# Performance work log

Measured on AMD Instinct MI355X. Metric: run time of the kernel, lower is better.

The kernel has to match this reference:

```python
import jax, jax.numpy as jnp
import numpy as np

N = 100000
E = 1600000
D_IN = 128
HEADS = 8
HEAD_DIM = 16  # hidden_channels // heads = 128 // 8
D_HID = HEADS * HEAD_DIM  # 128
D_OUT = 128
NEG_SLOPE = 0.2


def setup_inputs() -> dict:
    key = jax.random.key(0)
    ks = jax.random.split(key, 10)
    x = jax.random.normal(ks[0], (N, D_IN), dtype=jnp.float32)
    edge_index = jax.random.randint(ks[1], (2, E), 0, N, dtype=jnp.int64)
    s = 1.0 / np.sqrt(D_IN)
    W_gat = jax.random.uniform(ks[2], (D_IN, D_HID), minval=-s, maxval=s, dtype=jnp.float32)
    att_src = jax.random.uniform(ks[3], (HEADS, HEAD_DIM), minval=-s, maxval=s, dtype=jnp.float32)
    att_dst = jax.random.uniform(ks[4], (HEADS, HEAD_DIM), minval=-s, maxval=s, dtype=jnp.float32)
    b_gat = jnp.zeros((D_HID,), dtype=jnp.float32)
    so = 1.0 / np.sqrt(D_OUT)
    W_fc1 = jax.random.uniform(ks[5], (D_OUT, D_OUT), minval=-so, maxval=so, dtype=jnp.float32)
    b_fc1 = jax.random.uniform(ks[6], (D_OUT,), minval=-so, maxval=so, dtype=jnp.float32)
    W_fc2 = jax.random.uniform(ks[7], (D_OUT, D_OUT), minval=-so, maxval=so, dtype=jnp.float32)
    b_fc2 = jax.random.uniform(ks[8], (D_OUT,), minval=-so, maxval=so, dtype=jnp.float32)
    return {"x": x, "edge_index": edge_index, "W_gat": W_gat, "att_src": att_src,
            "att_dst": att_dst, "b_gat": b_gat, "W_fc1": W_fc1, "b_fc1": b_fc1,
            "W_fc2": W_fc2, "b_fc2": b_fc2}


def _gat_conv(x, src, dst, W_gat, att_src, att_dst, b_gat):
    n = x.shape[0]
    xp = (x @ W_gat).reshape(n, HEADS, HEAD_DIM)        # [N,H,C]
    a_src = jnp.einsum('nhc,hc->nh', xp, att_src)       # [N,H]
    a_dst = jnp.einsum('nhc,hc->nh', xp, att_dst)       # [N,H]
    e = jax.nn.leaky_relu(a_src[src] + a_dst[dst], NEG_SLOPE)  # [E,H]
    # segment softmax over edges grouped by destination node
    e_max = jax.ops.segment_max(e, dst, num_segments=n)
    e = jnp.exp(e - e_max[dst])
    e_sum = jax.ops.segment_sum(e, dst, num_segments=n)
    alpha = e / (e_sum[dst] + 1e-16)                    # [E,H]
    msg = xp[src] * alpha[:, :, None]                   # [E,H,C]
    out = jax.ops.segment_sum(msg, dst, num_segments=n) # [N,H,C]
    return out.reshape(n, D_HID) + b_gat


def reference(x, edge_index, W_gat, att_src, att_dst, b_gat, W_fc1, b_fc1, W_fc2, b_fc2):
    n = x.shape[0]
    # PyG GATConv default add_self_loops=True
    loops = jnp.arange(n, dtype=edge_index.dtype)
    src = jnp.concatenate([edge_index[0], loops])
    dst = jnp.concatenate([edge_index[1], loops])
    z = _gat_conv(x, src, dst, W_gat, att_src, att_dst, b_gat)
    z1 = z @ W_fc1 + b_fc1
    z2 = z @ W_fc2 + b_fc2
    return (z, z1, z2)
```

## Files before the change

kernel.cpp:

```cpp
#include <hip/hip_runtime.h>
#include <hip/hip_bf16.h>


#define NBUCK  256
#define BSHIFT 9
#define BNODES 512
#define IPB    8192

typedef __attribute__((ext_vector_type(8))) short bf16x8;
typedef __attribute__((ext_vector_type(4))) float f32x4;

static __device__ __forceinline__ short f2bf(float f) {
    __hip_bfloat16 h = __float2bfloat16(f);
    return *reinterpret_cast<short*>(&h);
}

__global__ __launch_bounds__(256) void k0_swizzle(
    const float* __restrict__ W0, const float* __restrict__ W1,
    const float* __restrict__ W2, unsigned short* __restrict__ S0,
    unsigned short* __restrict__ S1, unsigned short* __restrict__ S2)
{
    const int t = blockIdx.x * 256 + threadIdx.x;
    if (t >= 3 * 2048) return;
    const int m = t >> 11;
    const int r = t & 2047;
    const int tile = r >> 6;
    const int l    = r & 63;
    const int ks   = tile & 3;
    const int cb   = tile >> 2;
    const int c    = cb * 16 + (l & 15);
    const int kb   = ks * 32 + (l >> 4) * 8;
    const float* W = (m == 0) ? W0 : (m == 1) ? W1 : W2;
    unsigned short* S = (m == 0) ? S0 : (m == 1) ? S1 : S2;
    unsigned short* dst = S + ((size_t)tile * 64 + l) * 8;
#pragma unroll
    for (int j = 0; j < 8; ++j)
        dst[j] = (unsigned short)f2bf(W[(kb + j) * 128 + c]);
}

__global__ __launch_bounds__(256) void g1_mfma(
    const float* __restrict__ x, const unsigned short* __restrict__ Wswz,
    unsigned short* __restrict__ xpb, int n)
{
    const int wid  = __builtin_amdgcn_readfirstlane(threadIdx.x >> 6);
    const int lane = threadIdx.x & 63;
    const int lr   = lane & 15;
    const int kg   = lane >> 4;
    const int rowbase = blockIdx.x * 128 + wid * 32;

    bf16x8 afr[2][4];
#pragma unroll
    for (int rt = 0; rt < 2; ++rt) {
        int row = rowbase + rt * 16 + lr;
        row = (row < n) ? row : (n - 1);
        const float* rp = x + (size_t)row * 128 + kg * 8;
#pragma unroll
        for (int ks = 0; ks < 4; ++ks) {
            const float4 v0 = *reinterpret_cast<const float4*>(rp + ks * 32);
            const float4 v1 = *reinterpret_cast<const float4*>(rp + ks * 32 + 4);
            bf16x8 a;
            a[0] = f2bf(v0.x); a[1] = f2bf(v0.y); a[2] = f2bf(v0.z); a[3] = f2bf(v0.w);
            a[4] = f2bf(v1.x); a[5] = f2bf(v1.y); a[6] = f2bf(v1.z); a[7] = f2bf(v1.w);
            afr[rt][ks] = a;
        }
    }

    f32x4 acc[2][8] = {};
#pragma unroll
    for (int cb = 0; cb < 8; ++cb) {
        const unsigned short* bp = Wswz + ((size_t)(cb * 4) * 64 + lane) * 8;
        bf16x8 bfr[4];
#pragma unroll
        for (int ks = 0; ks < 4; ++ks)
            bfr[ks] = *reinterpret_cast<const bf16x8*>(bp + (size_t)ks * 512);
#pragma unroll
        for (int ks = 0; ks < 4; ++ks) {
            acc[0][cb] = __builtin_amdgcn_mfma_f32_16x16x32_bf16(afr[0][ks], bfr[ks], acc[0][cb], 0, 0, 0);
            acc[1][cb] = __builtin_amdgcn_mfma_f32_16x16x32_bf16(afr[1][ks], bfr[ks], acc[1][cb], 0, 0, 0);
        }
    }

#pragma unroll
    for (int rt = 0; rt < 2; ++rt) {
#pragma unroll
        for (int reg = 0; reg < 4; ++reg) {
            const int row = rowbase + rt * 16 + kg * 4 + reg;
            if (row < n) {
                unsigned short* op = xpb + (size_t)row * 128 + lr;
#pragma unroll
                for (int cb = 0; cb < 8; ++cb)
                    op[cb * 16] = (unsigned short)f2bf(acc[rt][cb][reg]);
            }
        }
    }
}

__global__ __launch_bounds__(256) void k1b_att(
    const unsigned short* __restrict__ xpb, const float* __restrict__ att_s,
    const float* __restrict__ att_d, float* __restrict__ a_src,
    float* __restrict__ a_dst, int n)
{
    const int tid  = threadIdx.x;
    const int col  = tid & 127;
    const int half = __builtin_amdgcn_readfirstlane(tid >> 7);
    const int rb   = blockIdx.x * 32 + half * 16;
    if (rb >= n) return;
    const float asw = att_s[col];
    const float adw = att_d[col];
    const int h = col >> 4;
#pragma unroll 4
    for (int r = 0; r < 16; ++r) {
        const int row = rb + r;
        if (row >= n) break;
        const unsigned int u = (unsigned int)xpb[(size_t)row * 128 + col] << 16;
        const float v = __uint_as_float(u);
        float sv = v * asw;
        float dv = v * adw;
#pragma unroll
        for (int off = 1; off < 16; off <<= 1) {
            sv += __shfl_xor(sv, off);
            dv += __shfl_xor(dv, off);
        }
        if ((col & 15) == 0) {
            a_src[row * 8 + h] = sv;
            a_dst[row * 8 + h] = dv;
        }
    }
}

__global__ __launch_bounds__(256) void p1_hist(
    const int* __restrict__ ei, int* __restrict__ M, int E, int N, int nblk)
{
    __shared__ int h[NBUCK];
    const int tid = threadIdx.x;
    for (int k = tid; k < NBUCK; k += 256) h[k] = 0;
    __syncthreads();

    const int tot = E + N;
    const int base = blockIdx.x * IPB;
    const int lim = (base + IPB < tot) ? base + IPB : tot;
    for (int j = base + tid; j < lim; j += 256) {
        const int d = (j < E) ? ei[E + j] : (j - E);
        atomicAdd(&h[d >> BSHIFT], 1);
    }
    __syncthreads();
    for (int k = tid; k < NBUCK; k += 256)
        M[(size_t)k * nblk + blockIdx.x] = h[k];
}

__global__ __launch_bounds__(256) void p2a_colscan(
    int* __restrict__ M, int* __restrict__ col_total, int nblk)
{
    const int b    = blockIdx.x;
    const int tid  = threadIdx.x;
    const int lane = tid & 63;
    const int wid  = tid >> 6;
    __shared__ int wsum[4];

    int carry = 0;
    for (int base = 0; base < nblk; base += 256) {
        const int idx = base + tid;
        const int v = (idx < nblk) ? M[(size_t)b * nblk + idx] : 0;
        int ws = v;
#pragma unroll
        for (int off = 1; off < 64; off <<= 1) {
            const int t = __shfl_up(ws, off);
            if (lane >= off) ws += t;
        }
        if (lane == 63) wsum[wid] = ws;
        __syncthreads();
        int woff = 0;
        for (int w2 = 0; w2 < wid; ++w2) woff += wsum[w2];
        const int alltot = wsum[0] + wsum[1] + wsum[2] + wsum[3];
        if (idx < nblk) M[(size_t)b * nblk + idx] = carry + woff + ws - v;
        carry += alltot;
        __syncthreads();
    }
    if (tid == 0) col_total[b] = carry;
}

__global__ __launch_bounds__(NBUCK) void p2b_bucketptr(
    const int* __restrict__ col_total, int* __restrict__ bucket_ptr,
    int* __restrict__ row_ptr, int N)
{
    const int tid  = threadIdx.x;
    const int lane = tid & 63;
    const int wid  = tid >> 6;
    __shared__ int wsum[4];

    const int v = col_total[tid];
    int ws = v;
#pragma unroll
    for (int off = 1; off < 64; off <<= 1) {
        const int t = __shfl_up(ws, off);
        if (lane >= off) ws += t;
    }
    if (lane == 63) wsum[wid] = ws;
    __syncthreads();
    int woff = 0;
    for (int w2 = 0; w2 < wid; ++w2) woff += wsum[w2];
    const int excl = woff + ws - v;
    bucket_ptr[tid] = excl;
    if (tid == NBUCK - 1) {
        bucket_ptr[NBUCK] = excl + v;
        row_ptr[N] = excl + v;
    }
}

__global__ __launch_bounds__(256) void p3_scatter(
    const int* __restrict__ ei, const int* __restrict__ M,
    const int* __restrict__ bucket_ptr, int2* __restrict__ pairs,
    int E, int N, int nblk)
{
    __shared__ int lcnt[NBUCK];
    const int tid = threadIdx.x;
    for (int k = tid; k < NBUCK; k += 256) lcnt[k] = 0;
    __syncthreads();

    const int tot = E + N;
    const int base = blockIdx.x * IPB;
    const int lim = (base + IPB < tot) ? base + IPB : tot;
    for (int j = base + tid; j < lim; j += 256) {
        int s, d;
        if (j < E) { s = ei[j]; d = ei[E + j]; }
        else       { s = j - E; d = s; }
        const int b = d >> BSHIFT;
        const int r = atomicAdd(&lcnt[b], 1);
        const int pos = bucket_ptr[b] + M[(size_t)b * nblk + blockIdx.x] + r;
        pairs[pos] = make_int2(s, d);
    }
}

__global__ __launch_bounds__(256) void p4_finalize(
    const int2* __restrict__ pairs, const int* __restrict__ bucket_ptr,
    int* __restrict__ row_ptr, int* __restrict__ csr_src, int N)
{
    const int b     = blockIdx.x;
    const int node0 = b << BSHIFT;
    const int beg   = bucket_ptr[b];
    const int end   = bucket_ptr[b + 1];
    const int tid   = threadIdx.x;
    const int lane  = tid & 63;
    const int wid   = tid >> 6;

    __shared__ int hist[BNODES];
    __shared__ int exc[BNODES];
    __shared__ int cnt2[BNODES];
    __shared__ int wsum[4];

    for (int k = tid; k < BNODES; k += 256) { hist[k] = 0; cnt2[k] = 0; }
    __syncthreads();

    for (int i = beg + tid; i < end; i += 256)
        atomicAdd(&hist[pairs[i].y - node0], 1);
    __syncthreads();

    const int a0 = hist[2 * tid];
    const int a1 = hist[2 * tid + 1];
    const int s  = a0 + a1;
    int ws = s;
#pragma unroll
    for (int off = 1; off < 64; off <<= 1) {
        const int t = __shfl_up(ws, off);
        if (lane >= off) ws += t;
    }
    if (lane == 63) wsum[wid] = ws;
    __syncthreads();
    int woff = 0;
    for (int w2 = 0; w2 < wid; ++w2) woff += wsum[w2];
    const int e0 = woff + ws - s;
    exc[2 * tid]     = e0;
    exc[2 * tid + 1] = e0 + a0;
    __syncthreads();

    for (int k = tid; k < BNODES; k += 256) {
        const int node = node0 + k;
        if (node < N) row_ptr[node] = beg + exc[k];
    }
    for (int i = beg + tid; i < end; i += 256) {
        const int2 p = pairs[i];
        const int dl = p.y - node0;
        const int r  = atomicAdd(&cnt2[dl], 1);
        csr_src[beg + exc[dl] + r] = p.x;
    }
}

__global__ __launch_bounds__(256) void k5_aggregate(
    const unsigned short* __restrict__ xpb, const float* __restrict__ a_src,
    const float* __restrict__ a_dst, const int* __restrict__ row_ptr,
    const int* __restrict__ csr_src, const float* __restrict__ b_gat,
    float* __restrict__ z, int n)
{
    const int wave = blockIdx.x * 4 + __builtin_amdgcn_readfirstlane(threadIdx.x >> 6);
    if (wave >= n) return;
    const int lane = threadIdx.x & 63;
    const int d = wave;
    const int beg = row_ptr[d];
    const int end = row_ptr[d + 1];
    const int h = lane >> 3;
    const float adst = a_dst[d * 8 + h];
    const int co = 2 * lane;

    float l0 = 0.f, l1 = 0.f;
    float ax0 = 0.f, ay0 = 0.f, ax1 = 0.f, ay1 = 0.f;

    int i = beg;
    for (; i + 4 <= end; i += 4) {
        const int s0 = csr_src[i + 0];
        const int s1 = csr_src[i + 1];
        const int s2 = csr_src[i + 2];
        const int s3 = csr_src[i + 3];
        const unsigned int xv0 = *reinterpret_cast<const unsigned int*>(xpb + (size_t)s0 * 128 + co);
        const unsigned int xv1 = *reinterpret_cast<const unsigned int*>(xpb + (size_t)s1 * 128 + co);
        const unsigned int xv2 = *reinterpret_cast<const unsigned int*>(xpb + (size_t)s2 * 128 + co);
        const unsigned int xv3 = *reinterpret_cast<const unsigned int*>(xpb + (size_t)s3 * 128 + co);
        float v0 = a_src[s0 * 8 + h] + adst;
        float v1 = a_src[s1 * 8 + h] + adst;
        float v2 = a_src[s2 * 8 + h] + adst;
        float v3 = a_src[s3 * 8 + h] + adst;
        v0 = (v0 > 0.f) ? v0 : 0.2f * v0;
        v1 = (v1 > 0.f) ? v1 : 0.2f * v1;
        v2 = (v2 > 0.f) ? v2 : 0.2f * v2;
        v3 = (v3 > 0.f) ? v3 : 0.2f * v3;
        const float p0 = __expf(v0);
        const float p1 = __expf(v1);
        const float p2 = __expf(v2);
        const float p3 = __expf(v3);
        l0 += p0 + p1;
        l1 += p2 + p3;
        ax0 = fmaf(p0, __uint_as_float(xv0 << 16), ax0);
        ay0 = fmaf(p0, __uint_as_float(xv0 & 0xffff0000u), ay0);
        ax1 = fmaf(p1, __uint_as_float(xv1 << 16), ax1);
        ay1 = fmaf(p1, __uint_as_float(xv1 & 0xffff0000u), ay1);
        ax0 = fmaf(p2, __uint_as_float(xv2 << 16), ax0);
        ay0 = fmaf(p2, __uint_as_float(xv2 & 0xffff0000u), ay0);
        ax1 = fmaf(p3, __uint_as_float(xv3 << 16), ax1);
        ay1 = fmaf(p3, __uint_as_float(xv3 & 0xffff0000u), ay1);
    }
    for (; i < end; ++i) {
        const int s = csr_src[i];
        const unsigned int xv = *reinterpret_cast<const unsigned int*>(xpb + (size_t)s * 128 + co);
        float v = a_src[s * 8 + h] + adst;
        v = (v > 0.f) ? v : 0.2f * v;
        const float p = __expf(v);
        l0 += p;
        ax0 = fmaf(p, __uint_as_float(xv << 16), ax0);
        ay0 = fmaf(p, __uint_as_float(xv & 0xffff0000u), ay0);
    }

    const float inv = 1.0f / (l0 + l1 + 1e-16f);
    const float2 bg = *reinterpret_cast<const float2*>(&b_gat[co]);
    float2 o;
    o.x = (ax0 + ax1) * inv + bg.x;
    o.y = (ay0 + ay1) * inv + bg.y;
    *reinterpret_cast<float2*>(&z[(size_t)d * 128 + co]) = o;
}

__global__ __launch_bounds__(256) void g2_mfma_fc(
    const float* __restrict__ z,
    const unsigned short* __restrict__ S1, const unsigned short* __restrict__ S2,
    const float* __restrict__ b1, const float* __restrict__ b2,
    float* __restrict__ z1, float* __restrict__ z2, int n)
{
    const int wid  = __builtin_amdgcn_readfirstlane(threadIdx.x >> 6);
    const int lane = threadIdx.x & 63;
    const int lr   = lane & 15;
    const int kg   = lane >> 4;
    const int rowbase = blockIdx.x * 128 + wid * 32;

    bf16x8 afr[2][4];
#pragma unroll
    for (int rt = 0; rt < 2; ++rt) {
        int row = rowbase + rt * 16 + lr;
        row = (row < n) ? row : (n - 1);
        const float* rp = z + (size_t)row * 128 + kg * 8;
#pragma unroll
        for (int ks = 0; ks < 4; ++ks) {
            const float4 v0 = *reinterpret_cast<const float4*>(rp + ks * 32);
            const float4 v1 = *reinterpret_cast<const float4*>(rp + ks * 32 + 4);
            bf16x8 a;
            a[0] = f2bf(v0.x); a[1] = f2bf(v0.y); a[2] = f2bf(v0.z); a[3] = f2bf(v0.w);
            a[4] = f2bf(v1.x); a[5] = f2bf(v1.y); a[6] = f2bf(v1.z); a[7] = f2bf(v1.w);
            afr[rt][ks] = a;
        }
    }

    f32x4 acc1[2][8] = {};
    f32x4 acc2[2][8] = {};
#pragma unroll
    for (int cb = 0; cb < 8; ++cb) {
        const unsigned short* bp1 = S1 + ((size_t)(cb * 4) * 64 + lane) * 8;
        const unsigned short* bp2 = S2 + ((size_t)(cb * 4) * 64 + lane) * 8;
        bf16x8 f1[4], f2v[4];
#pragma unroll
        for (int ks = 0; ks < 4; ++ks) {
            f1[ks]  = *reinterpret_cast<const bf16x8*>(bp1 + (size_t)ks * 512);
            f2v[ks] = *reinterpret_cast<const bf16x8*>(bp2 + (size_t)ks * 512);
        }
#pragma unroll
        for (int ks = 0; ks < 4; ++ks) {
            acc1[0][cb] = __builtin_amdgcn_mfma_f32_16x16x32_bf16(afr[0][ks], f1[ks],  acc1[0][cb], 0, 0, 0);
            acc1[1][cb] = __builtin_amdgcn_mfma_f32_16x16x32_bf16(afr[1][ks], f1[ks],  acc1[1][cb], 0, 0, 0);
            acc2[0][cb] = __builtin_amdgcn_mfma_f32_16x16x32_bf16(afr[0][ks], f2v[ks], acc2[0][cb], 0, 0, 0);
            acc2[1][cb] = __builtin_amdgcn_mfma_f32_16x16x32_bf16(afr[1][ks], f2v[ks], acc2[1][cb], 0, 0, 0);
        }
    }

    float bb1[8], bb2[8];
#pragma unroll
    for (int cb = 0; cb < 8; ++cb) { bb1[cb] = b1[cb * 16 + lr]; bb2[cb] = b2[cb * 16 + lr]; }

#pragma unroll
    for (int rt = 0; rt < 2; ++rt) {
#pragma unroll
        for (int reg = 0; reg < 4; ++reg) {
            const int row = rowbase + rt * 16 + kg * 4 + reg;
            if (row < n) {
                float* o1 = z1 + (size_t)row * 128 + lr;
                float* o2 = z2 + (size_t)row * 128 + lr;
#pragma unroll
                for (int cb = 0; cb < 8; ++cb) {
                    o1[cb * 16] = acc1[rt][cb][reg] + bb1[cb];
                    o2[cb * 16] = acc2[rt][cb][reg] + bb2[cb];
                }
            }
        }
    }
}

extern "C" void kernel_launch(void* const* d_in, const int* in_sizes, int n_in,
                              void* d_out, int out_size, void* d_ws, size_t ws_size,
                              hipStream_t stream)
{
    const float* x       = (const float*)d_in[0];
    const int*   ei      = (const int*)  d_in[1];
    const float* W_gat   = (const float*)d_in[2];
    const float* att_src = (const float*)d_in[3];
    const float* att_dst = (const float*)d_in[4];
    const float* b_gat   = (const float*)d_in[5];
    const float* W_fc1   = (const float*)d_in[6];
    const float* b_fc1   = (const float*)d_in[7];
    const float* W_fc2   = (const float*)d_in[8];
    const float* b_fc2   = (const float*)d_in[9];

    const int N = in_sizes[0] / 128;
    const int E = in_sizes[1] / 2;
    const int tot = E + N;
    const int nblk = (tot + IPB - 1) / IPB;
    const int nbuck_used = (N + BNODES - 1) >> BSHIFT;

    char* w = (char*)d_ws;
    unsigned short* xpb = (unsigned short*)w;  w += (size_t)N * 128 * 2;
    float* a_src  = (float*)w;  w += (size_t)N * 8 * 4;
    float* a_dst  = (float*)w;  w += (size_t)N * 8 * 4;
    int* row_ptr  = (int*)w;    w += (size_t)(N + 1) * 4;
    w = (char*)(((size_t)w + 15) & ~(size_t)15);
    unsigned short* S0 = (unsigned short*)w; w += 16384 * 2;
    unsigned short* S1 = (unsigned short*)w; w += 16384 * 2;
    unsigned short* S2 = (unsigned short*)w; w += 16384 * 2;
    int* M          = (int*)w;  w += (size_t)nblk * NBUCK * 4;
    int* col_total  = (int*)w;  w += NBUCK * 4;
    int* bucket_ptr = (int*)w;  w += (NBUCK + 1) * 4;
    w = (char*)(((size_t)w + 15) & ~(size_t)15);
    int2* pairs   = (int2*)w;   w += (size_t)tot * 8;
    int* csr_src  = (int*)w;    w += (size_t)tot * 4;

    float* z  = (float*)d_out;
    float* z1 = z  + (size_t)N * 128;
    float* z2 = z1 + (size_t)N * 128;

    k0_swizzle<<<(3 * 2048 + 255) / 256, 256, 0, stream>>>(W_gat, W_fc1, W_fc2, S0, S1, S2);

    g1_mfma<<<(N + 127) / 128, 256, 0, stream>>>(x, S0, xpb, N);
    k1b_att<<<(N + 31) / 32, 256, 0, stream>>>(xpb, att_src, att_dst, a_src, a_dst, N);

    p1_hist<<<nblk, 256, 0, stream>>>(ei, M, E, N, nblk);
    p2a_colscan<<<NBUCK, 256, 0, stream>>>(M, col_total, nblk);
    p2b_bucketptr<<<1, NBUCK, 0, stream>>>(col_total, bucket_ptr, row_ptr, N);
    p3_scatter<<<nblk, 256, 0, stream>>>(ei, M, bucket_ptr, pairs, E, N, nblk);
    p4_finalize<<<nbuck_used, 256, 0, stream>>>(pairs, bucket_ptr, row_ptr, csr_src, N);

    k5_aggregate<<<(N + 3) / 4, 256, 0, stream>>>(xpb, a_src, a_dst, row_ptr, csr_src,
                                                  b_gat, z, N);

    g2_mfma_fc<<<(N + 127) / 128, 256, 0, stream>>>(z, S1, S2, b_fc1, b_fc2, z1, z2, N);
}
```

Before: 238.9 us.

## Fold attention projections into GEMM, pack CSR pairs, emit bf16 z for FC

Precomputes W_gat·att_src/att_dst as an extra bf16 B-tile so g1_mfma computes a_src/a_dst with four extra MFMAs per row tile, removing the separate k1b_att kernel and its reread of xpb. Packs each (src, local dst) pair into one 32-bit int, halving the pairs buffer traffic in scatter and finalize. k5_aggregate also writes a bf16 copy of z, which g2 reads instead of converting fp32 z. The trade-offs are a slight change in numerics, since attention logits now come from bf16 W·att products, and a source-index limit of 17 bits.

```diff
diff --git a/kernel.cpp b/kernel.cpp
--- a/kernel.cpp
+++ b/kernel.cpp
@@ -17,30 +17,51 @@
 
 __global__ __launch_bounds__(256) void k0_swizzle(
     const float* __restrict__ W0, const float* __restrict__ W1,
-    const float* __restrict__ W2, unsigned short* __restrict__ S0,
-    unsigned short* __restrict__ S1, unsigned short* __restrict__ S2)
+    const float* __restrict__ W2, const float* __restrict__ att_s,
+    const float* __restrict__ att_d, unsigned short* __restrict__ S0,
+    unsigned short* __restrict__ S1, unsigned short* __restrict__ S2,
+    unsigned short* __restrict__ Sa)
 {
     const int t = blockIdx.x * 256 + threadIdx.x;
-    if (t >= 3 * 2048) return;
-    const int m = t >> 11;
-    const int r = t & 2047;
-    const int tile = r >> 6;
-    const int l    = r & 63;
-    const int ks   = tile & 3;
-    const int cb   = tile >> 2;
-    const int c    = cb * 16 + (l & 15);
-    const int kb   = ks * 32 + (l >> 4) * 8;
-    const float* W = (m == 0) ? W0 : (m == 1) ? W1 : W2;
-    unsigned short* S = (m == 0) ? S0 : (m == 1) ? S1 : S2;
-    unsigned short* dst = S + ((size_t)tile * 64 + l) * 8;
-#pragma unroll
-    for (int j = 0; j < 8; ++j)
-        dst[j] = (unsigned short)f2bf(W[(kb + j) * 128 + c]);
+    if (t < 3 * 2048) {
+        const int m = t >> 11;
+        const int r = t & 2047;
+        const int tile = r >> 6;
+        const int l    = r & 63;
+        const int ks   = tile & 3;
+        const int cb   = tile >> 2;
+        const int c    = cb * 16 + (l & 15);
+        const int kb   = ks * 32 + (l >> 4) * 8;
+        const float* W = (m == 0) ? W0 : (m == 1) ? W1 : W2;
+        unsigned short* S = (m == 0) ? S0 : (m == 1) ? S1 : S2;
+        unsigned short* dst = S + ((size_t)tile * 64 + l) * 8;
+#pragma unroll
+        for (int j = 0; j < 8; ++j)
+            dst[j] = (unsigned short)f2bf(W[(kb + j) * 128 + c]);
+    } else if (t < 3 * 2048 + 256) {
+        const int r  = t - 3 * 2048;
+        const int ks = r >> 6;
+        const int l  = r & 63;
+        const int hp = l & 15;
+        const int h  = hp & 7;
+        const float* av = (hp < 8) ? (att_s + h * 16) : (att_d + h * 16);
+        unsigned short* dst = Sa + ((size_t)ks * 64 + l) * 8;
+#pragma unroll
+        for (int j = 0; j < 8; ++j) {
+            const int k = ks * 32 + (l >> 4) * 8 + j;
+            float acc = 0.f;
+#pragma unroll
+            for (int u = 0; u < 16; ++u)
+                acc += W0[k * 128 + h * 16 + u] * av[u];
+            dst[j] = (unsigned short)f2bf(acc);
+        }
+    }
 }
 
 __global__ __launch_bounds__(256) void g1_mfma(
     const float* __restrict__ x, const unsigned short* __restrict__ Wswz,
-    unsigned short* __restrict__ xpb, int n)
+    const unsigned short* __restrict__ Sa, unsigned short* __restrict__ xpb,
+    float* __restrict__ a_src, float* __restrict__ a_dst, int n)
 {
     const int wid  = __builtin_amdgcn_readfirstlane(threadIdx.x >> 6);
     const int lane = threadIdx.x & 63;
@@ -80,6 +101,14 @@
         }
     }
 
+    f32x4 accs[2] = {};
+#pragma unroll
+    for (int ks = 0; ks < 4; ++ks) {
+        const bf16x8 bs = *reinterpret_cast<const bf16x8*>(Sa + ((size_t)ks * 64 + lane) * 8);
+        accs[0] = __builtin_amdgcn_mfma_f32_16x16x32_bf16(afr[0][ks], bs, accs[0], 0, 0, 0);
+        accs[1] = __builtin_amdgcn_mfma_f32_16x16x32_bf16(afr[1][ks], bs, accs[1], 0, 0, 0);
+    }
+
 #pragma unroll
     for (int rt = 0; rt < 2; ++rt) {
 #pragma unroll
@@ -90,40 +119,9 @@
 #pragma unroll
                 for (int cb = 0; cb < 8; ++cb)
                     op[cb * 16] = (unsigned short)f2bf(acc[rt][cb][reg]);
+                if (lr < 8) a_src[row * 8 + lr] = accs[rt][reg];
+                else        a_dst[row * 8 + (lr - 8)] = accs[rt][reg];
             }
-        }
-    }
-}
-
-__global__ __launch_bounds__(256) void k1b_att(
-    const unsigned short* __restrict__ xpb, const float* __restrict__ att_s,
-    const float* __restrict__ att_d, float* __restrict__ a_src,
-    float* __restrict__ a_dst, int n)
-{
-    const int tid  = threadIdx.x;
-    const int col  = tid & 127;
-    const int half = __builtin_amdgcn_readfirstlane(tid >> 7);
-    const int rb   = blockIdx.x * 32 + half * 16;
-    if (rb >= n) return;
-    const float asw = att_s[col];
-    const float adw = att_d[col];
-    const int h = col >> 4;
-#pragma unroll 4
-    for (int r = 0; r < 16; ++r) {
-        const int row = rb + r;
-        if (row >= n) break;
-        const unsigned int u = (unsigned int)xpb[(size_t)row * 128 + col] << 16;
-        const float v = __uint_as_float(u);
-        float sv = v * asw;
-        float dv = v * adw;
-#pragma unroll
-        for (int off = 1; off < 16; off <<= 1) {
-            sv += __shfl_xor(sv, off);
-            dv += __shfl_xor(dv, off);
-        }
-        if ((col & 15) == 0) {
-            a_src[row * 8 + h] = sv;
-            a_dst[row * 8 + h] = dv;
         }
     }
 }
@@ -209,7 +207,7 @@
 
 __global__ __launch_bounds__(256) void p3_scatter(
     const int* __restrict__ ei, const int* __restrict__ M,
-    const int* __restrict__ bucket_ptr, int2* __restrict__ pairs,
+    const int* __restrict__ bucket_ptr, int* __restrict__ pairs,
     int E, int N, int nblk)
 {
     __shared__ int lcnt[NBUCK];
@@ -227,12 +225,12 @@
         const int b = d >> BSHIFT;
         const int r = atomicAdd(&lcnt[b], 1);
         const int pos = bucket_ptr[b] + M[(size_t)b * nblk + blockIdx.x] + r;
-        pairs[pos] = make_int2(s, d);
+        pairs[pos] = s | ((d & (BNODES - 1)) << 17);
     }
 }
 
 __global__ __launch_bounds__(256) void p4_finalize(
-    const int2* __restrict__ pairs, const int* __restrict__ bucket_ptr,
+    const int* __restrict__ pairs, const int* __restrict__ bucket_ptr,
     int* __restrict__ row_ptr, int* __restrict__ csr_src, int N)
 {
     const int b     = blockIdx.x;
@@ -252,7 +250,7 @@
     __syncthreads();
 
     for (int i = beg + tid; i < end; i += 256)
-        atomicAdd(&hist[pairs[i].y - node0], 1);
+        atomicAdd(&hist[pairs[i] >> 17], 1);
     __syncthreads();
 
     const int a0 = hist[2 * tid];
@@ -278,10 +276,10 @@
         if (node < N) row_ptr[node] = beg + exc[k];
     }
     for (int i = beg + tid; i < end; i += 256) {
-        const int2 p = pairs[i];
-        const int dl = p.y - node0;
+        const int v  = pairs[i];
+        const int dl = v >> 17;
         const int r  = atomicAdd(&cnt2[dl], 1);
-        csr_src[beg + exc[dl] + r] = p.x;
+        csr_src[beg + exc[dl] + r] = v & 0x1FFFF;
     }
 }
 
@@ -289,7 +287,7 @@
     const unsigned short* __restrict__ xpb, const float* __restrict__ a_src,
     const float* __restrict__ a_dst, const int* __restrict__ row_ptr,
     const int* __restrict__ csr_src, const float* __restrict__ b_gat,
-    float* __restrict__ z, int n)
+    float* __restrict__ z, unsigned int* __restrict__ zb, int n)
 {
     const int wave = blockIdx.x * 4 + __builtin_amdgcn_readfirstlane(threadIdx.x >> 6);
     if (wave >= n) return;
@@ -354,10 +352,13 @@
     o.x = (ax0 + ax1) * inv + bg.x;
     o.y = (ay0 + ay1) * inv + bg.y;
     *reinterpret_cast<float2*>(&z[(size_t)d * 128 + co]) = o;
+    const unsigned int pk = ((unsigned int)(unsigned short)f2bf(o.y) << 16) |
+                            (unsigned int)(unsigned short)f2bf(o.x);
+    zb[(size_t)d * 64 + lane] = pk;
 }
 
 __global__ __launch_bounds__(256) void g2_mfma_fc(
-    const float* __restrict__ z,
+    const unsigned int* __restrict__ zb,
     const unsigned short* __restrict__ S1, const unsigned short* __restrict__ S2,
     const float* __restrict__ b1, const float* __restrict__ b2,
     float* __restrict__ z1, float* __restrict__ z2, int n)
@@ -373,16 +374,10 @@
     for (int rt = 0; rt < 2; ++rt) {
         int row = rowbase + rt * 16 + lr;
         row = (row < n) ? row : (n - 1);
-        const float* rp = z + (size_t)row * 128 + kg * 8;
-#pragma unroll
-        for (int ks = 0; ks < 4; ++ks) {
-            const float4 v0 = *reinterpret_cast<const float4*>(rp + ks * 32);
-            const float4 v1 = *reinterpret_cast<const float4*>(rp + ks * 32 + 4);
-            bf16x8 a;
-            a[0] = f2bf(v0.x); a[1] = f2bf(v0.y); a[2] = f2bf(v0.z); a[3] = f2bf(v0.w);
-            a[4] = f2bf(v1.x); a[5] = f2bf(v1.y); a[6] = f2bf(v1.z); a[7] = f2bf(v1.w);
-            afr[rt][ks] = a;
-        }
+        const unsigned short* rp = (const unsigned short*)(zb + (size_t)row * 64) + kg * 8;
+#pragma unroll
+        for (int ks = 0; ks < 4; ++ks)
+            afr[rt][ks] = *reinterpret_cast<const bf16x8*>(rp + ks * 32);
     }
 
     f32x4 acc1[2][8] = {};
@@ -451,6 +446,7 @@
 
     char* w = (char*)d_ws;
     unsigned short* xpb = (unsigned short*)w;  w += (size_t)N * 128 * 2;
+    unsigned int* zb = (unsigned int*)w;       w += (size_t)N * 64 * 4;
     float* a_src  = (float*)w;  w += (size_t)N * 8 * 4;
     float* a_dst  = (float*)w;  w += (size_t)N * 8 * 4;
     int* row_ptr  = (int*)w;    w += (size_t)(N + 1) * 4;
@@ -458,21 +454,22 @@
     unsigned short* S0 = (unsigned short*)w; w += 16384 * 2;
     unsigned short* S1 = (unsigned short*)w; w += 16384 * 2;
     unsigned short* S2 = (unsigned short*)w; w += 16384 * 2;
+    unsigned short* Sa = (unsigned short*)w; w += 2048 * 2;
     int* M          = (int*)w;  w += (size_t)nblk * NBUCK * 4;
     int* col_total  = (int*)w;  w += NBUCK * 4;
     int* bucket_ptr = (int*)w;  w += (NBUCK + 1) * 4;
     w = (char*)(((size_t)w + 15) & ~(size_t)15);
-    int2* pairs   = (int2*)w;   w += (size_t)tot * 8;
+    int* pairs    = (int*)w;    w += (size_t)tot * 4;
     int* csr_src  = (int*)w;    w += (size_t)tot * 4;
 
     float* z  = (float*)d_out;
     float* z1 = z  + (size_t)N * 128;
     float* z2 = z1 + (size_t)N * 128;
 
-    k0_swizzle<<<(3 * 2048 + 255) / 256, 256, 0, stream>>>(W_gat, W_fc1, W_fc2, S0, S1, S2);
-
-    g1_mfma<<<(N + 127) / 128, 256, 0, stream>>>(x, S0, xpb, N);
-    k1b_att<<<(N + 31) / 32, 256, 0, stream>>>(xpb, att_src, att_dst, a_src, a_dst, N);
+    k0_swizzle<<<(3 * 2048 + 256 + 255) / 256, 256, 0, stream>>>(
+        W_gat, W_fc1, W_fc2, att_src, att_dst, S0, S1, S2, Sa);
+
+    g1_mfma<<<(N + 127) / 128, 256, 0, stream>>>(x, S0, Sa, xpb, a_src, a_dst, N);
 
     p1_hist<<<nblk, 256, 0, stream>>>(ei, M, E, N, nblk);
     p2a_colscan<<<NBUCK, 256, 0, stream>>>(M, col_total, nblk);
@@ -481,7 +478,7 @@
     p4_finalize<<<nbuck_used, 256, 0, stream>>>(pairs, bucket_ptr, row_ptr, csr_src, N);
 
     k5_aggregate<<<(N + 3) / 4, 256, 0, stream>>>(xpb, a_src, a_dst, row_ptr, csr_src,
-                                                  b_gat, z, N);
-
-    g2_mfma_fc<<<(N + 127) / 128, 256, 0, stream>>>(z, S1, S2, b_fc1, b_fc2, z1, z2, N);
-}
+                                                  b_gat, z, zb, N);
+
+    g2_mfma_fc<<<(N + 127) / 128, 256, 0, stream>>>(zb, S1, S2, b_fc1, b_fc2, z1, z2, N);
+}
```

Result: faster. 218.7 us (-8.4%).
